# Performance work log

Hardware: AMD Instinct MI355X
Metric: run time of the kernel (lower is better)

The kernel has to match this reference:

```python
import jax, jax.numpy as jnp
import numpy as np

B, N, D_U = 32, 4096, 64
D = 128          # mlp_dim == model dim after MLP
H = 2            # n_heads
DH = D // H


def setup_inputs() -> dict:
    key = jax.random.key(0)
    ks = jax.random.split(key, 16)
    sc = lambda fan_in: 1.0 / np.sqrt(fan_in)
    inp = {
        "u": jax.random.normal(ks[0], (B, N, D_U), dtype=jnp.float32),
        "x": jax.random.uniform(ks[1], (B, N, 2), dtype=jnp.float32),
        # MLP params: [D_U -> D -> D], gelu after each hidden layer
        "W1": jax.random.normal(ks[2], (D_U, D), dtype=jnp.float32) * sc(D_U),
        "b1": jnp.zeros((D,), jnp.float32),
        "W2": jax.random.normal(ks[3], (D, D), dtype=jnp.float32) * sc(D),
        "b2": jnp.zeros((D,), jnp.float32),
        # learned pooling query (nn.Embed(1, D))
        "embed": jax.random.normal(ks[4], (1, D), dtype=jnp.float32),
        # multihead linear attention projections
        "Wq": jax.random.normal(ks[5], (D, D), dtype=jnp.float32) * sc(D),
        "bq": jnp.zeros((D,), jnp.float32),
        "Wk": jax.random.normal(ks[6], (D, D), dtype=jnp.float32) * sc(D),
        "bk": jnp.zeros((D,), jnp.float32),
        "Wv": jax.random.normal(ks[7], (D, D), dtype=jnp.float32) * sc(D),
        "bv": jnp.zeros((D,), jnp.float32),
        "Wo": jax.random.normal(ks[8], (D, D), dtype=jnp.float32) * sc(D),
        "bo": jnp.zeros((D,), jnp.float32),
    }
    return inp


def reference(u, x, W1, b1, W2, b2, embed, Wq, bq, Wk, bk, Wv, bv, Wo, bo):
    # MLP on set elements: [B, N, D_U] -> [B, N, D]
    z = jax.nn.gelu(u @ W1 + b1)
    z = jax.nn.gelu(z @ W2 + b2)

    n = z.shape[1]
    # learned query broadcast over batch: [B, 1, D]
    s = jnp.broadcast_to(embed[None, :, :], (z.shape[0], 1, z.shape[-1]))

    # multihead linear (Galerkin-style, softmax-free) attention
    q = (s @ Wq + bq).reshape(z.shape[0], 1, H, DH)   # [B, 1, H, DH]
    k = (z @ Wk + bk).reshape(z.shape[0], n, H, DH)   # [B, N, H, DH]
    v = (z @ Wv + bv).reshape(z.shape[0], n, H, DH)   # [B, N, H, DH]

    # context = K^T V / N per head: [B, H, DH, DH]
    context = jnp.einsum("bnhd,bnhe->bhde", k, v) / n
    out = jnp.einsum("bqhd,bhde->bqhe", q, context)   # [B, 1, H, DH]
    out = out.reshape(z.shape[0], 1, D) @ Wo + bo     # [B, 1, D]

    return out[:, 0, :]                               # [B, D]
```

## Files before the change

kernel.cpp:

```cpp
#include <hip/hip_runtime.h>
#include <math.h>

#define Bsz 32
#define Nn  4096
#define DU  64
#define Dm  128

#define GRID_MLP 512
#define BPB 16

#define WS_WKQ 0
#define WS_BKQ 256
#define WS_CNT 288
#define WS_A   320
#define WS_S   384
#define WS_WP  8576

#define H1STR 136

typedef short frag_ab __attribute__((ext_vector_type(8)));
typedef float frag_cd __attribute__((ext_vector_type(4)));

__device__ __forceinline__ unsigned short f2bf(float x) {
    union { float f; unsigned int u; } c; c.f = x;
    unsigned int r = c.u + 0x7fffu + ((c.u >> 16) & 1u);
    return (unsigned short)(r >> 16);
}

__device__ __forceinline__ float gelu_fast(float x) {
    float t = x * x;
    float a = x * fmaf(t, -0.1029432f, -2.3022081f);
    float e = __builtin_amdgcn_exp2f(a);
    return x * __builtin_amdgcn_rcpf(1.0f + e);
}

__global__ __launch_bounds__(256) void precompute_kernel(
    const float* __restrict__ embed, const float* __restrict__ Wq,
    const float* __restrict__ bq, const float* __restrict__ Wk,
    const float* __restrict__ bk, const float* __restrict__ W1,
    const float* __restrict__ W2, float* __restrict__ ws)
{
    __shared__ float qv[128];
    const int tid = threadIdx.x;
    const int bid = blockIdx.x;

    if (bid < 12) {
        const int e = bid * 256 + tid;
        const int f = e >> 6, L = e & 63;
        const int q2 = L >> 4, n = L & 15;
        const float* src;
        int ks, nt;
        if (f < 16) { src = W1; ks = f >> 3;        nt = f & 7; }
        else        { src = W2; ks = (f - 16) >> 3; nt = (f - 16) & 7; }
        const int kb = ks * 32 + q2 * 8;
        const int c  = nt * 16 + n;
        unsigned int p[4];
        #pragma unroll
        for (int jj = 0; jj < 4; ++jj) {
            unsigned int lo = f2bf(src[(kb + 2 * jj)     * Dm + c]);
            unsigned int hi = f2bf(src[(kb + 2 * jj + 1) * Dm + c]);
            p[jj] = lo | (hi << 16);
        }
        ((uint4*)(ws + WS_WP))[e] = make_uint4(p[0], p[1], p[2], p[3]);
    } else if (bid == 12) {
        if (tid < 128) {
            float s = bq[tid];
            #pragma unroll 8
            for (int j = 0; j < 128; ++j) s += embed[j] * Wq[j * 128 + tid];
            qv[tid] = s;
        }
        __syncthreads();
        if (tid < 128) {
            float s0 = 0.f, s1 = 0.f;
            #pragma unroll 8
            for (int dh = 0; dh < 64; ++dh) {
                s0 += Wk[tid * 128 + dh]      * qv[dh];
                s1 += Wk[tid * 128 + 64 + dh] * qv[64 + dh];
            }
            ws[WS_WKQ + tid]       = s0;
            ws[WS_WKQ + 128 + tid] = s1;
        }
        if (tid < 2) {
            float s = 0.f;
            for (int dh = 0; dh < 64; ++dh) s += bk[tid * 64 + dh] * qv[tid * 64 + dh];
            ws[WS_BKQ + tid] = s;
        }
    } else {
        for (int idx = WS_CNT + tid; idx < WS_WP; idx += 256) ws[idx] = 0.f;
    }
}

__global__ __launch_bounds__(512) void mlp_pool_kernel(
    const float* __restrict__ u,  const float* __restrict__ b1,
    const float* __restrict__ b2, const float* __restrict__ Wv,
    const float* __restrict__ bv, const float* __restrict__ Wo,
    const float* __restrict__ bo, float* __restrict__ ws,
    float* __restrict__ out)
{
    __shared__ short lds_w[48 * 512];
    __shared__ short lds_h1[4 * 16 * H1STR];
    __shared__ float a2buf[4][16][2][2];
    __shared__ int   do_epi;

    const int tid  = threadIdx.x;
    const int wave = tid >> 6;
    const int lane = tid & 63;
    const int quad = lane >> 4;
    const int n15  = lane & 15;
    const int p    = wave >> 1;
    const int hf   = wave & 1;

    {
        const float4* src = (const float4*)(ws + WS_WP);
        float4* dst = (float4*)lds_w;
        #pragma unroll
        for (int i = 0; i < 6; ++i) dst[tid + 512 * i] = src[tid + 512 * i];
    }

    float b1c[4], b2c[4], wkq0[4], wkq1[4];
    #pragma unroll
    for (int nt = 0; nt < 4; ++nt) {
        const int c = hf * 64 + nt * 16 + n15;
        b1c[nt]  = b1[c];
        b2c[nt]  = b2[c];
        wkq0[nt] = ws[WS_WKQ + c];
        wkq1[nt] = ws[WS_WKQ + 128 + c];
    }
    const float bkq0 = ws[WS_BKQ];
    const float bkq1 = ws[WS_BKQ + 1];
    __syncthreads();

    const int bb = blockIdx.x >> 4;
    const int jb = blockIdx.x & 15;
    short* h1t = lds_h1 + p * 16 * H1STR;

    float s0p[4], s1p[4];
    #pragma unroll
    for (int nt = 0; nt < 4; ++nt) { s0p[nt] = 0.f; s1p[nt] = 0.f; }
    float aA0 = 0.f, aA1 = 0.f;

    const float* ub = u + ((size_t)(bb * Nn + jb * 256 + p * 16 + n15)) * DU + quad * 8;
    float4 f0 = *(const float4*)(ub);
    float4 f1 = *(const float4*)(ub + 4);
    float4 f2 = *(const float4*)(ub + 32);
    float4 f3 = *(const float4*)(ub + 36);

    #pragma unroll 1
    for (int it = 0; it < 4; ++it) {
        frag_ab a0, a1;
        a0[0] = (short)f2bf(f0.x); a0[1] = (short)f2bf(f0.y);
        a0[2] = (short)f2bf(f0.z); a0[3] = (short)f2bf(f0.w);
        a0[4] = (short)f2bf(f1.x); a0[5] = (short)f2bf(f1.y);
        a0[6] = (short)f2bf(f1.z); a0[7] = (short)f2bf(f1.w);
        a1[0] = (short)f2bf(f2.x); a1[1] = (short)f2bf(f2.y);
        a1[2] = (short)f2bf(f2.z); a1[3] = (short)f2bf(f2.w);
        a1[4] = (short)f2bf(f3.x); a1[5] = (short)f2bf(f3.y);
        a1[6] = (short)f2bf(f3.z); a1[7] = (short)f2bf(f3.w);

        if (it < 3) {
            const float* un = ub + (size_t)((it + 1) * 64) * DU;
            f0 = *(const float4*)(un);
            f1 = *(const float4*)(un + 4);
            f2 = *(const float4*)(un + 32);
            f3 = *(const float4*)(un + 36);
        }

        frag_cd acc[4];
        #pragma unroll
        for (int nt = 0; nt < 4; ++nt) acc[nt] = (frag_cd){0.f, 0.f, 0.f, 0.f};
        #pragma unroll
        for (int nt = 0; nt < 4; ++nt) {
            const int f = hf * 4 + nt;
            frag_ab w0 = *(const frag_ab*)&lds_w[(f)     * 512 + lane * 8];
            acc[nt] = __builtin_amdgcn_mfma_f32_16x16x32_bf16(a0, w0, acc[nt], 0, 0, 0);
            frag_ab w1 = *(const frag_ab*)&lds_w[(8 + f) * 512 + lane * 8];
            acc[nt] = __builtin_amdgcn_mfma_f32_16x16x32_bf16(a1, w1, acc[nt], 0, 0, 0);
        }

        #pragma unroll
        for (int nt = 0; nt < 4; ++nt) {
            #pragma unroll
            for (int r = 0; r < 4; ++r) {
                float g = gelu_fast(acc[nt][r] + b1c[nt]);
                h1t[(quad * 4 + r) * H1STR + hf * 64 + nt * 16 + n15] = (short)f2bf(g);
            }
        }
        __syncthreads();

        frag_cd acc2[4];
        #pragma unroll
        for (int nt = 0; nt < 4; ++nt) acc2[nt] = (frag_cd){0.f, 0.f, 0.f, 0.f};
        #pragma unroll
        for (int ks = 0; ks < 4; ++ks) {
            frag_ab a2 = *(const frag_ab*)&h1t[n15 * H1STR + ks * 32 + quad * 8];
            #pragma unroll
            for (int nt = 0; nt < 4; ++nt) {
                frag_ab w2f = *(const frag_ab*)&lds_w[(16 + ks * 8 + hf * 4 + nt) * 512 + lane * 8];
                acc2[nt] = __builtin_amdgcn_mfma_f32_16x16x32_bf16(a2, w2f, acc2[nt], 0, 0, 0);
            }
        }

        #pragma unroll
        for (int nt = 0; nt < 4; ++nt) {
            #pragma unroll
            for (int r = 0; r < 4; ++r)
                acc2[nt][r] = gelu_fast(acc2[nt][r] + b2c[nt]);
        }

        float p0[4], p1[4];
        #pragma unroll
        for (int r = 0; r < 4; ++r) { p0[r] = 0.f; p1[r] = 0.f; }
        #pragma unroll
        for (int nt = 0; nt < 4; ++nt) {
            #pragma unroll
            for (int r = 0; r < 4; ++r) {
                p0[r] += acc2[nt][r] * wkq0[nt];
                p1[r] += acc2[nt][r] * wkq1[nt];
            }
        }
        #pragma unroll
        for (int r = 0; r < 4; ++r) {
            #pragma unroll
            for (int d = 1; d < 16; d <<= 1) {
                p0[r] += __shfl_xor(p0[r], d);
                p1[r] += __shfl_xor(p1[r], d);
            }
        }
        if (n15 == 0) {
            #pragma unroll
            for (int r = 0; r < 4; ++r) {
                const int row = quad * 4 + r;
                a2buf[p][row][0][hf] = p0[r];
                a2buf[p][row][1][hf] = p1[r];
            }
        }
        __syncthreads();

        #pragma unroll
        for (int r = 0; r < 4; ++r) {
            const int row = quad * 4 + r;
            const float al0 = a2buf[p][row][0][0] + a2buf[p][row][0][1] + bkq0;
            const float al1 = a2buf[p][row][1][0] + a2buf[p][row][1][1] + bkq1;
            #pragma unroll
            for (int nt = 0; nt < 4; ++nt) {
                s0p[nt] += al0 * acc2[nt][r];
                s1p[nt] += al1 * acc2[nt][r];
            }
            aA0 += al0; aA1 += al1;
        }
    }

    #pragma unroll
    for (int nt = 0; nt < 4; ++nt) {
        s0p[nt] += __shfl_xor(s0p[nt], 16); s0p[nt] += __shfl_xor(s0p[nt], 32);
        s1p[nt] += __shfl_xor(s1p[nt], 16); s1p[nt] += __shfl_xor(s1p[nt], 32);
    }
    aA0 += __shfl_xor(aA0, 16); aA0 += __shfl_xor(aA0, 32);
    aA1 += __shfl_xor(aA1, 16); aA1 += __shfl_xor(aA1, 32);

    if (quad == 0) {
        #pragma unroll
        for (int nt = 0; nt < 4; ++nt) {
            const int c = hf * 64 + nt * 16 + n15;
            atomicAdd(&ws[WS_S + (bb * 2 + 0) * 128 + c], s0p[nt]);
            atomicAdd(&ws[WS_S + (bb * 2 + 1) * 128 + c], s1p[nt]);
        }
    }
    if (hf == 0 && lane == 0) {
        atomicAdd(&ws[WS_A + bb * 2 + 0], aA0);
        atomicAdd(&ws[WS_A + bb * 2 + 1], aA1);
    }

    __syncthreads();
    if (tid == 0) {
        __threadfence();
        int old = atomicAdd((int*)ws + WS_CNT + bb, 1);
        do_epi = (old == BPB - 1) ? 1 : 0;
    }
    __syncthreads();

    if (do_epi) {
        float* eb     = (float*)lds_h1;
        float* e_sS   = eb;
        float* e_sA   = eb + 256;
        float* e_pool = eb + 264;
        float* e_part = eb + 392;

        if (tid < 256) e_sS[tid] = atomicAdd(&ws[WS_S + bb * 256 + tid], 0.f);
        if (tid < 2)   e_sA[tid] = atomicAdd(&ws[WS_A + bb * 2 + tid], 0.f);
        __syncthreads();

        const int i = tid & 127, seg = tid >> 7;
        const int h = i >> 6;
        {
            float dot = 0.f;
            #pragma unroll 8
            for (int d0 = 0; d0 < 32; ++d0) {
                const int d = seg * 32 + d0;
                dot += e_sS[h * 128 + d] * Wv[d * 128 + i];
            }
            e_part[tid] = dot;
        }
        __syncthreads();
        if (tid < 128)
            e_pool[i] = (e_part[i] + e_part[128 + i] + e_part[256 + i] + e_part[384 + i]
                         + e_sA[h] * bv[i]) * (1.0f / 4096.0f);
        __syncthreads();

        {
            float o = 0.f;
            #pragma unroll 8
            for (int d0 = 0; d0 < 32; ++d0) {
                const int d = seg * 32 + d0;
                o += e_pool[d] * Wo[d * 128 + i];
            }
            e_part[tid] = o;
        }
        __syncthreads();
        if (tid < 128)
            out[bb * 128 + i] = bo[i] + e_part[i] + e_part[128 + i] + e_part[256 + i] + e_part[384 + i];
    }
}

extern "C" void kernel_launch(void* const* d_in, const int* in_sizes, int n_in,
                              void* d_out, int out_size, void* d_ws, size_t ws_size,
                              hipStream_t stream) {
    const float* u     = (const float*)d_in[0];
    const float* W1    = (const float*)d_in[2];
    const float* b1    = (const float*)d_in[3];
    const float* W2    = (const float*)d_in[4];
    const float* b2    = (const float*)d_in[5];
    const float* embed = (const float*)d_in[6];
    const float* Wq    = (const float*)d_in[7];
    const float* bq    = (const float*)d_in[8];
    const float* Wk    = (const float*)d_in[9];
    const float* bk    = (const float*)d_in[10];
    const float* Wv    = (const float*)d_in[11];
    const float* bv    = (const float*)d_in[12];
    const float* Wo    = (const float*)d_in[13];
    const float* bo    = (const float*)d_in[14];
    float* ws  = (float*)d_ws;
    float* out = (float*)d_out;

    hipLaunchKernelGGL(precompute_kernel, dim3(14), dim3(256), 0, stream,
                       embed, Wq, bq, Wk, bk, W1, W2, ws);
    hipLaunchKernelGGL(mlp_pool_kernel, dim3(GRID_MLP), dim3(512), 0, stream,
                       u, b1, b2, Wv, bv, Wo, bo, ws, out);
}
```

Measured before the change: 147.9 us.

## Shrink blocks to 256 threads, hold W2 fragments in registers, quadruple grid

The MLP kernel moves from 512 blocks of 512 threads to 2048 blocks of 256 threads, each block handling 64 rows over two iterations. Each wave now keeps its W2 MFMA fragments in registers loaded straight from global memory, and only W1 is staged in LDS. This cuts LDS use per block and removes LDS reads from the second matmul, aiming at higher occupancy and better latency hiding. In exchange it drops the software prefetch of the next u tile, uses more registers per thread, quadruples the per-block W1 staging and atomic traffic, and makes the epilogue's reductions run over 64 rows per thread.

```diff
diff --git a/kernel.cpp b/kernel.cpp
--- a/kernel.cpp
+++ b/kernel.cpp
@@ -6,8 +6,8 @@
 #define DU  64
 #define Dm  128
 
-#define GRID_MLP 512
-#define BPB 16
+#define GRID_MLP 2048
+#define BPB 64
 
 #define WS_WKQ 0
 #define WS_BKQ 256
@@ -90,16 +90,16 @@
     }
 }
 
-__global__ __launch_bounds__(512) void mlp_pool_kernel(
+__global__ __launch_bounds__(256) void mlp_pool_kernel(
     const float* __restrict__ u,  const float* __restrict__ b1,
     const float* __restrict__ b2, const float* __restrict__ Wv,
     const float* __restrict__ bv, const float* __restrict__ Wo,
     const float* __restrict__ bo, float* __restrict__ ws,
     float* __restrict__ out)
 {
-    __shared__ short lds_w[48 * 512];
-    __shared__ short lds_h1[4 * 16 * H1STR];
-    __shared__ float a2buf[4][16][2][2];
+    __shared__ short lds_w1[16 * 512];
+    __shared__ short lds_h1[2 * 16 * H1STR];
+    __shared__ float a2buf[2][16][2][2];
     __shared__ int   do_epi;
 
     const int tid  = threadIdx.x;
@@ -110,11 +110,19 @@
     const int p    = wave >> 1;
     const int hf   = wave & 1;
 
+    const short* wst = (const short*)(ws + WS_WP) + lane * 8;
+    frag_ab w2r[16];
+    #pragma unroll
+    for (int i = 0; i < 16; ++i) {
+        const int ks = i >> 2, nt = i & 3;
+        w2r[i] = *(const frag_ab*)(wst + (16 + ks * 8 + hf * 4 + nt) * 512);
+    }
+
     {
         const float4* src = (const float4*)(ws + WS_WP);
-        float4* dst = (float4*)lds_w;
-        #pragma unroll
-        for (int i = 0; i < 6; ++i) dst[tid + 512 * i] = src[tid + 512 * i];
+        float4* dst = (float4*)lds_w1;
+        #pragma unroll
+        for (int i = 0; i < 4; ++i) dst[tid + 256 * i] = src[tid + 256 * i];
     }
 
     float b1c[4], b2c[4], wkq0[4], wkq1[4];
@@ -130,8 +138,8 @@
     const float bkq1 = ws[WS_BKQ + 1];
     __syncthreads();
 
-    const int bb = blockIdx.x >> 4;
-    const int jb = blockIdx.x & 15;
+    const int bb = blockIdx.x >> 6;
+    const int jb = blockIdx.x & 63;
     short* h1t = lds_h1 + p * 16 * H1STR;
 
     float s0p[4], s1p[4];
@@ -139,14 +147,14 @@
     for (int nt = 0; nt < 4; ++nt) { s0p[nt] = 0.f; s1p[nt] = 0.f; }
     float aA0 = 0.f, aA1 = 0.f;
 
-    const float* ub = u + ((size_t)(bb * Nn + jb * 256 + p * 16 + n15)) * DU + quad * 8;
-    float4 f0 = *(const float4*)(ub);
-    float4 f1 = *(const float4*)(ub + 4);
-    float4 f2 = *(const float4*)(ub + 32);
-    float4 f3 = *(const float4*)(ub + 36);
-
     #pragma unroll 1
-    for (int it = 0; it < 4; ++it) {
+    for (int it = 0; it < 2; ++it) {
+        const float* up = u + ((size_t)(bb * Nn + jb * 64 + it * 32 + p * 16 + n15)) * DU + quad * 8;
+        float4 f0 = *(const float4*)(up);
+        float4 f1 = *(const float4*)(up + 4);
+        float4 f2 = *(const float4*)(up + 32);
+        float4 f3 = *(const float4*)(up + 36);
+
         frag_ab a0, a1;
         a0[0] = (short)f2bf(f0.x); a0[1] = (short)f2bf(f0.y);
         a0[2] = (short)f2bf(f0.z); a0[3] = (short)f2bf(f0.w);
@@ -157,23 +165,15 @@
         a1[4] = (short)f2bf(f3.x); a1[5] = (short)f2bf(f3.y);
         a1[6] = (short)f2bf(f3.z); a1[7] = (short)f2bf(f3.w);
 
-        if (it < 3) {
-            const float* un = ub + (size_t)((it + 1) * 64) * DU;
-            f0 = *(const float4*)(un);
-            f1 = *(const float4*)(un + 4);
-            f2 = *(const float4*)(un + 32);
-            f3 = *(const float4*)(un + 36);
-        }
-
         frag_cd acc[4];
         #pragma unroll
         for (int nt = 0; nt < 4; ++nt) acc[nt] = (frag_cd){0.f, 0.f, 0.f, 0.f};
         #pragma unroll
         for (int nt = 0; nt < 4; ++nt) {
             const int f = hf * 4 + nt;
-            frag_ab w0 = *(const frag_ab*)&lds_w[(f)     * 512 + lane * 8];
+            frag_ab w0 = *(const frag_ab*)&lds_w1[(f)     * 512 + lane * 8];
             acc[nt] = __builtin_amdgcn_mfma_f32_16x16x32_bf16(a0, w0, acc[nt], 0, 0, 0);
-            frag_ab w1 = *(const frag_ab*)&lds_w[(8 + f) * 512 + lane * 8];
+            frag_ab w1 = *(const frag_ab*)&lds_w1[(8 + f) * 512 + lane * 8];
             acc[nt] = __builtin_amdgcn_mfma_f32_16x16x32_bf16(a1, w1, acc[nt], 0, 0, 0);
         }
 
@@ -195,8 +195,7 @@
             frag_ab a2 = *(const frag_ab*)&h1t[n15 * H1STR + ks * 32 + quad * 8];
             #pragma unroll
             for (int nt = 0; nt < 4; ++nt) {
-                frag_ab w2f = *(const frag_ab*)&lds_w[(16 + ks * 8 + hf * 4 + nt) * 512 + lane * 8];
-                acc2[nt] = __builtin_amdgcn_mfma_f32_16x16x32_bf16(a2, w2f, acc2[nt], 0, 0, 0);
+                acc2[nt] = __builtin_amdgcn_mfma_f32_16x16x32_bf16(a2, w2r[ks * 4 + nt], acc2[nt], 0, 0, 0);
             }
         }
 
@@ -286,8 +285,8 @@
         float* e_pool = eb + 264;
         float* e_part = eb + 392;
 
-        if (tid < 256) e_sS[tid] = atomicAdd(&ws[WS_S + bb * 256 + tid], 0.f);
-        if (tid < 2)   e_sA[tid] = atomicAdd(&ws[WS_A + bb * 2 + tid], 0.f);
+        e_sS[tid] = atomicAdd(&ws[WS_S + bb * 256 + tid], 0.f);
+        if (tid < 2) e_sA[tid] = atomicAdd(&ws[WS_A + bb * 2 + tid], 0.f);
         __syncthreads();
 
         const int i = tid & 127, seg = tid >> 7;
@@ -295,30 +294,29 @@
         {
             float dot = 0.f;
             #pragma unroll 8
-            for (int d0 = 0; d0 < 32; ++d0) {
-                const int d = seg * 32 + d0;
+            for (int d0 = 0; d0 < 64; ++d0) {
+                const int d = seg * 64 + d0;
                 dot += e_sS[h * 128 + d] * Wv[d * 128 + i];
             }
             e_part[tid] = dot;
         }
         __syncthreads();
         if (tid < 128)
-            e_pool[i] = (e_part[i] + e_part[128 + i] + e_part[256 + i] + e_part[384 + i]
-                         + e_sA[h] * bv[i]) * (1.0f / 4096.0f);
+            e_pool[i] = (e_part[i] + e_part[128 + i] + e_sA[h] * bv[i]) * (1.0f / 4096.0f);
         __syncthreads();
 
         {
             float o = 0.f;
             #pragma unroll 8
-            for (int d0 = 0; d0 < 32; ++d0) {
-                const int d = seg * 32 + d0;
+            for (int d0 = 0; d0 < 64; ++d0) {
+                const int d = seg * 64 + d0;
                 o += e_pool[d] * Wo[d * 128 + i];
             }
             e_part[tid] = o;
         }
         __syncthreads();
         if (tid < 128)
-            out[bb * 128 + i] = bo[i] + e_part[i] + e_part[128 + i] + e_part[256 + i] + e_part[384 + i];
+            out[bb * 128 + i] = bo[i] + e_part[i] + e_part[128 + i];
     }
 }
 
@@ -344,6 +342,6 @@
 
     hipLaunchKernelGGL(precompute_kernel, dim3(14), dim3(256), 0, stream,
                        embed, Wq, bq, Wk, bk, W1, W2, ws);
-    hipLaunchKernelGGL(mlp_pool_kernel, dim3(GRID_MLP), dim3(512), 0, stream,
+    hipLaunchKernelGGL(mlp_pool_kernel, dim3(GRID_MLP), dim3(256), 0, stream,
                        u, b1, b2, Wv, bv, Wo, bo, ws, out);
 }
```

Measured after the change: 210.5 us. 1.42x slower.
